# Optimization experiments

Hardware: AMD Instinct MI355X
Metric: run time of the kernel (lower is better)

## Reference

```python
import jax, jax.numpy as jnp
import numpy as np

G, K1, K2, N, NP, EPS = 16, 128, 32, 128, 512, 1e-5

def _bn(x, axes):
    m = jnp.mean(x, axes, keepdims=True)
    v = jnp.var(x, axes, keepdims=True)  # biased, as torch BN training mode
    return (x - m) * jax.lax.rsqrt(v + EPS)

def _fps(xyz, npoint):
    # farthest point sampling, deterministic start at index 0; xyz (B,P,3)
    B, P, _ = xyz.shape
    def step(carry, _):
        dists, far = carry
        c = jnp.take_along_axis(xyz, far[:, None, None], axis=1)   # (B,1,3)
        d = jnp.sum((xyz - c) ** 2, -1)                            # (B,P)
        dists = jnp.minimum(dists, d)
        return (dists, jnp.argmax(dists, -1)), far
    init = (jnp.full((B, P), 1e10, xyz.dtype), jnp.zeros((B,), jnp.int32))
    _, idx = jax.lax.scan(step, init, None, length=npoint)         # (npoint,B)
    return jnp.take_along_axis(xyz, idx.T[:, :, None], axis=1)     # (B,npoint,3)

def _pointnet(x, w1, b1, w2, b2, w3, b3):
    h = jax.nn.relu(_bn(x @ w1 + b1, (0, 1)))
    h = jax.nn.relu(_bn(h @ w2 + b2, (0, 1)))
    h = _bn(h @ w3 + b3, (0, 1))
    return jnp.max(h, axis=1)                                      # (B,1024)

def _mapping(feat, w1, b1, w2, b2, w3, b3, w4, b4):
    # all 16 branches stacked on leading axis g
    h = jax.nn.relu(_bn(jnp.einsum('bk,gkj->gbj', feat, w1) + b1[:, None, :], (1,)))
    h = jax.nn.relu(_bn(jnp.einsum('gbj,gjk->gbk', h, w2) + b2[:, None, :], (1,)))
    h = jax.nn.relu(_bn(jnp.einsum('gbj,gjk->gbk', h, w3) + b3[:, None, :], (1,)))
    return jax.nn.relu(_bn(jnp.einsum('gbj,gjk->gbk', h, w4) + b4[:, None, :], (1,)))

def _axform(feat, fw, fb, c1w, c1b, c2w, c2b, c3w, c3b, c4w, c4b):
    # feat (G,B,K1); 1x1 convs expressed as einsums in channels-last layout
    xb = (jnp.einsum('gbk,gkm->gbm', feat, fw) + fb[:, None, :]).reshape(G, -1, N, K2)
    h = jax.nn.relu(_bn(jnp.einsum('gbnk,gkc->gbnc', xb, c1w) + c1b[:, None, None, :], (1, 2)))
    h = jax.nn.relu(_bn(jnp.einsum('gbnc,gcd->gbnd', h, c2w) + c2b[:, None, None, :], (1, 2)))
    h = jnp.einsum('gbnd,gde->gbne', h, c3w) + c3b[:, None, None, :]  # (G,B,N,1024)
    w = jax.nn.softmax(h, axis=2)                                     # softmax over N
    y = jnp.einsum('gbne,gbnk->gbek', w, xb)                          # (G,B,1024,K2)
    return jnp.einsum('gbek,gkc->gbec', y, c4w) + c4b[:, None, None, :]  # (G,B,1024,3)

def _forward(x, pn, mp, gen, ref):
    x_partial = _fps(x, NP)                                           # (B,512,3)
    feat = _pointnet(x, *pn)                                          # (B,1024)
    mfeat = _mapping(feat, *mp)                                       # (G,B,K1)
    x1g = _axform(mfeat, *gen)                                        # (G,B,1024,3)
    B = x.shape[0]
    x_1 = jnp.transpose(x1g, (1, 0, 2, 3)).reshape(B, -1, 3)          # (B,16384,3)
    fps1 = jax.vmap(lambda p: _fps(p, NP))(x1g)                       # (G,B,512,3)
    x_base = jnp.concatenate([fps1, jnp.broadcast_to(x_partial, (G,) + x_partial.shape)], axis=2)
    x2g = x_base + _axform(mfeat, *ref)                               # (G,B,1024,3)
    x_2 = jnp.transpose(x2g, (1, 0, 2, 3)).reshape(B, -1, 3)
    return x_1, x_2

def setup_inputs() -> dict:
    keys = iter(jax.random.split(jax.random.key(0), 40))
    def rn(shape, s=0.02):
        return (s * jax.random.normal(next(keys), shape)).astype(jnp.float32)
    inp = {}
    inp['x'] = jax.random.normal(next(keys), (16, 2048, 3), jnp.float32)
    inp['pn_w1'] = rn((3, 64));      inp['pn_b1'] = rn((64,))
    inp['pn_w2'] = rn((64, 128));    inp['pn_b2'] = rn((128,))
    inp['pn_w3'] = rn((128, 1024));  inp['pn_b3'] = rn((1024,))
    inp['mp_w1'] = rn((G, 1024, 1024)); inp['mp_b1'] = rn((G, 1024))
    inp['mp_w2'] = rn((G, 1024, 1024)); inp['mp_b2'] = rn((G, 1024))
    inp['mp_w3'] = rn((G, 1024, 1024)); inp['mp_b3'] = rn((G, 1024))
    inp['mp_w4'] = rn((G, 1024, K1));   inp['mp_b4'] = rn((G, K1))
    for p in ('g', 'r'):
        inp[p + '_fw'] = rn((G, K1, N * K2)); inp[p + '_fb'] = rn((G, N * K2))
        inp[p + '_c1w'] = rn((G, K2, 64));    inp[p + '_c1b'] = rn((G, 64))
        inp[p + '_c2w'] = rn((G, 64, 128));   inp[p + '_c2b'] = rn((G, 128))
        inp[p + '_c3w'] = rn((G, 128, 1024)); inp[p + '_c3b'] = rn((G, 1024))
        inp[p + '_c4w'] = rn((G, K2, 3));     inp[p + '_c4b'] = rn((G, 3))
    return inp

def reference(x, pn_w1, pn_b1, pn_w2, pn_b2, pn_w3, pn_b3,
              mp_w1, mp_b1, mp_w2, mp_b2, mp_w3, mp_b3, mp_w4, mp_b4,
              g_fw, g_fb, g_c1w, g_c1b, g_c2w, g_c2b, g_c3w, g_c3b, g_c4w, g_c4b,
              r_fw, r_fb, r_c1w, r_c1b, r_c2w, r_c2b, r_c3w, r_c3b, r_c4w, r_c4b):
    pn = (pn_w1, pn_b1, pn_w2, pn_b2, pn_w3, pn_b3)
    mp = (mp_w1, mp_b1, mp_w2, mp_b2, mp_w3, mp_b3, mp_w4, mp_b4)
    gen = (g_fw, g_fb, g_c1w, g_c1b, g_c2w, g_c2b, g_c3w, g_c3b, g_c4w, g_c4b)
    ref = (r_fw, r_fb, r_c1w, r_c1b, r_c2w, r_c2b, r_c3w, r_c3b, r_c4w, r_c4b)
    return _forward(x, pn, mp, gen, ref)
```

## Files before the change

### kernel.cpp

```cpp
#include <hip/hip_runtime.h>
#include <math.h>

#define TID ((int)threadIdx.x)

namespace {
constexpr float EPSf = 1e-5f;

typedef __attribute__((ext_vector_type(8))) short short8;
typedef __attribute__((ext_vector_type(4))) float f32x4;

struct FpsArgs {
  const float* pts; float* out; float* dmin; int* far;
  int it0, it1, nc;
};

__device__ __forceinline__ unsigned fenc(float f){
  unsigned u = __float_as_uint(f);
  return (u & 0x80000000u) ? ~u : (u | 0x80000000u);
}
__device__ __forceinline__ float fdec(unsigned e){
  unsigned u = (e & 0x80000000u) ? (e & 0x7fffffffu) : ~e;
  return __uint_as_float(u);
}
__device__ __forceinline__ short bf16rne(float f){
  unsigned u = __float_as_uint(f);
  return (short)((u + 0x7fffu + ((u >> 16) & 1u)) >> 16);
}

template<int CTRL>
__device__ __forceinline__ void dpp_comb(float& bm, int& bp){
  int om_i = __builtin_amdgcn_update_dpp(__float_as_int(bm), __float_as_int(bm), CTRL, 0xf, 0xf, false);
  int op   = __builtin_amdgcn_update_dpp(bp, bp, CTRL, 0xf, 0xf, false);
  float om = __int_as_float(om_i);
  if (om > bm || (om == bm && op < bp)){ bm = om; bp = op; }
}

template<int LP, int NT>
__device__ void fps_body(const FpsArgs& a, int ci){
  const int NPTS = NT*LP;
  const float* pts = a.pts + (size_t)ci * NPTS * 3;
  float* out = a.out + (size_t)ci * 512 * 3;
  float* dst = a.dmin + (size_t)ci * NPTS;
  float px[LP], py[LP], pz[LP], dmin[LP];
#pragma unroll
  for (int j = 0; j < LP; j++){
    int p = TID + NT*j;
    px[j] = pts[p*3+0]; py[j] = pts[p*3+1]; pz[j] = pts[p*3+2];
  }
  int far;
  if (a.it0 == 0){
#pragma unroll
    for (int j = 0; j < LP; j++) dmin[j] = 1e10f;
    far = 0;
  } else {
#pragma unroll
    for (int j = 0; j < LP; j++) dmin[j] = dst[TID + NT*j];
    far = a.far[ci];
  }
  __shared__ unsigned long long red2[2][NT/64];
  for (int i = a.it0; i < a.it1; i++){
    float cx = pts[far*3+0], cy = pts[far*3+1], cz = pts[far*3+2];
    if (TID == 0){ out[i*3+0]=cx; out[i*3+1]=cy; out[i*3+2]=cz; }
    float bm = -1.f; int bp = 0;
#pragma unroll
    for (int j = 0; j < LP; j++){
      float dx = __fsub_rn(px[j], cx);
      float dy = __fsub_rn(py[j], cy);
      float dz = __fsub_rn(pz[j], cz);
      float d  = __fadd_rn(__fadd_rn(__fmul_rn(dx,dx), __fmul_rn(dy,dy)), __fmul_rn(dz,dz));
      float dm = fminf(dmin[j], d);
      dmin[j] = dm;
      if (dm > bm){ bm = dm; bp = TID + NT*j; }
    }
    dpp_comb<0x111>(bm,bp); dpp_comb<0x112>(bm,bp); dpp_comb<0x114>(bm,bp);
    dpp_comb<0x118>(bm,bp); dpp_comb<0x142>(bm,bp); dpp_comb<0x143>(bm,bp);
    unsigned long long key =
      ((unsigned long long)(unsigned)__builtin_amdgcn_readlane(__float_as_int(bm), 63) << 32)
      | (unsigned)~(unsigned)__builtin_amdgcn_readlane(bp, 63);
    if ((TID & 63) == 63) red2[i&1][TID>>6] = key;
    __syncthreads();
    unsigned long long kk = red2[i&1][0];
#pragma unroll
    for (int t = 1; t < NT/64; t++){
      unsigned long long o = red2[i&1][t];
      kk = kk > o ? kk : o;
    }
    far = (int)~(unsigned)kk;
  }
  if (a.it1 < 512){
#pragma unroll
    for (int j = 0; j < LP; j++) dst[TID + NT*j] = dmin[j];
    if (TID == 0) a.far[ci] = far;
  }
}

__device__ __forceinline__ int pswz(int n, int e){
  return (n << 6) + (e ^ (((n >> 3) & 3) << 3) ^ ((n >> 5) & 3));
}

template<int C, int K, int FLP>
__global__ void __launch_bounds__(256) rowgemm_kernel(const float* __restrict__ in,
    const float* __restrict__ w, const float* __restrict__ bias, const float2* __restrict__ st2,
    float* __restrict__ out, int rows_per_g, FpsArgs fa)
{
  int bid = blockIdx.x;
  if constexpr (FLP > 0){
    if (bid < fa.nc){ fps_body<FLP,256>(fa, bid); return; }
    bid -= fa.nc;
  }
  constexpr int RPB = 256 / C;
  __shared__ float lin[RPB * K];
  size_t row0 = (size_t)bid * RPB;
  int g = (int)(row0 / rows_per_g);
  for (int i = TID; i < RPB*K; i += 256){
    float v = in[row0*(size_t)K + i];
    if (st2){ float2 s = st2[(size_t)g*K + (i % K)]; v = fmaxf((v - s.x)*s.y, 0.f); }
    lin[i] = v;
  }
  __syncthreads();
  int r = TID / C, c = TID % C;
  float acc = bias[(size_t)g*C + c];
  const float* wg = w + (size_t)g*K*C + c;
#pragma unroll
  for (int k = 0; k < K; k++) acc = fmaf(lin[r*K + k], wg[(size_t)k*C], acc);
  out[(row0 + r)*C + c] = acc;
}

template<int FLP>
__global__ void __launch_bounds__(256, 4) big1024b_kernel(const float* __restrict__ in,
    const float* __restrict__ w, const float* __restrict__ bias, const float2* __restrict__ st2,
    float* __restrict__ ps, float* __restrict__ pq, unsigned* __restrict__ maxenc, FpsArgs fa)
{
  int bid = blockIdx.x;
  if constexpr (FLP > 0){
    if (bid < fa.nc){ fps_body<FLP,256>(fa, bid); return; }
    bid -= fa.nc;
  }
  int rb = bid >> 1, ch = bid & 1;
  size_t row0 = (size_t)rb * 32;
  __shared__ float linT[4096];
  for (int i = TID; i < 4096; i += 256){
    int r = i >> 7, k = i & 127;
    float v = in[(row0 + r)*128 + k];
    float2 s = st2[k];
    linT[k*32 + r] = fmaxf((v - s.x)*s.y, 0.f);
  }
  __syncthreads();
  int rq = TID >> 6, cq = TID & 63;
  int c0 = ch*512 + cq*8;
  float acc[8][8];
  {
    float4 b0 = *(const float4*)(bias + c0);
    float4 b1 = *(const float4*)(bias + c0 + 4);
    const float bv[8] = {b0.x,b0.y,b0.z,b0.w,b1.x,b1.y,b1.z,b1.w};
#pragma unroll
    for (int ri = 0; ri < 8; ri++)
#pragma unroll
      for (int ci = 0; ci < 8; ci++) acc[ri][ci] = bv[ci];
  }
  const float* wp = w + c0;
#pragma unroll 2
  for (int k = 0; k < 128; k++){
    float4 w0 = *(const float4*)(wp + (size_t)k*1024);
    float4 w1 = *(const float4*)(wp + (size_t)k*1024 + 4);
    float4 l0 = *(const float4*)&linT[k*32 + rq*8];
    float4 l1 = *(const float4*)&linT[k*32 + rq*8 + 4];
    const float lv[8] = {l0.x,l0.y,l0.z,l0.w,l1.x,l1.y,l1.z,l1.w};
    const float wv[8] = {w0.x,w0.y,w0.z,w0.w,w1.x,w1.y,w1.z,w1.w};
#pragma unroll
    for (int ri = 0; ri < 8; ri++)
#pragma unroll
      for (int ci = 0; ci < 8; ci++)
        acc[ri][ci] = fmaf(lv[ri], wv[ci], acc[ri][ci]);
  }
  float s[8], q[8], m[8];
#pragma unroll
  for (int ci = 0; ci < 8; ci++){
    s[ci] = 0.f; q[ci] = 0.f; m[ci] = -1e38f;
#pragma unroll
    for (int ri = 0; ri < 8; ri++){
      float v = acc[ri][ci];
      s[ci] += v; q[ci] = fmaf(v, v, q[ci]); m[ci] = fmaxf(m[ci], v);
    }
  }
  __syncthreads();
  float* red = linT;
#pragma unroll
  for (int ci = 0; ci < 8; ci++){
    red[rq*512 + cq*8 + ci]        = s[ci];
    red[2048 + rq*512 + cq*8 + ci] = q[ci];
  }
  __syncthreads();
  if (rq == 0){
#pragma unroll
    for (int ci = 0; ci < 8; ci++){
      float ss = 0.f, qq = 0.f;
#pragma unroll
      for (int r = 0; r < 4; r++){
        ss += red[r*512 + cq*8 + ci];
        qq += red[2048 + r*512 + cq*8 + ci];
      }
      ps[(size_t)rb*1024 + c0 + ci] = ss;
      pq[(size_t)rb*1024 + c0 + ci] = qq;
    }
  }
  __syncthreads();
#pragma unroll
  for (int ci = 0; ci < 8; ci++) red[rq*512 + cq*8 + ci] = m[ci];
  __syncthreads();
  if (rq == 0){
    int b = (int)(row0 / 2048);
#pragma unroll
    for (int ci = 0; ci < 8; ci++){
      float mm = red[cq*8 + ci];
#pragma unroll
      for (int r = 1; r < 4; r++) mm = fmaxf(mm, red[r*512 + cq*8 + ci]);
      atomicMax(&maxenc[(size_t)b*1024 + c0 + ci], fenc(mm));
    }
  }
}

template<int FLP>
__global__ void __launch_bounds__(128) mapgemm2_kernel(const float* __restrict__ in, int in_gstride,
    const float* __restrict__ w, const float* __restrict__ bias, const float2* __restrict__ st2,
    float* __restrict__ out, int K, int J, int JB, int NS, FpsArgs fa)
{
  int bid = blockIdx.x;
  if constexpr (FLP > 0){
    if (bid < fa.nc){ fps_body<FLP,128>(fa, bid); return; }
    bid -= fa.nc;
  }
  int kc = bid / (JB*16);
  int g  = (bid / JB) % 16;
  int jb = bid % JB;
  int kchunk = K / NS, k0 = kc*kchunk;
  __shared__ float linT[128*16];
  const float* ing = in + (size_t)g * in_gstride;
  for (int i = TID; i < kchunk*16; i += 128){
    int b = i / kchunk, k = i - b*kchunk;
    float v = ing[(size_t)b*K + k0 + k];
    if (st2){ float2 s = st2[(size_t)g*K + k0 + k]; v = fmaxf((v - s.x)*s.y, 0.f); }
    linT[k*16 + b] = v;
  }
  __syncthreads();
  int bh = TID >> 6, jq = TID & 63;
  int j = jb*256 + jq*4;
  const float* wp = w + ((size_t)g*K + k0)*J + j;
  float4 a4[8];
#pragma unroll
  for (int bi = 0; bi < 8; bi++) a4[bi] = make_float4(0.f,0.f,0.f,0.f);
#pragma unroll 4
  for (int k = 0; k < kchunk; k++){
    float4 wv = *(const float4*)(wp + (size_t)k*J);
    float4 l0 = *(const float4*)&linT[k*16 + bh*8];
    float4 l1 = *(const float4*)&linT[k*16 + bh*8 + 4];
    const float lv[8] = {l0.x,l0.y,l0.z,l0.w,l1.x,l1.y,l1.z,l1.w};
#pragma unroll
    for (int bi = 0; bi < 8; bi++){
      a4[bi].x = fmaf(lv[bi], wv.x, a4[bi].x);
      a4[bi].y = fmaf(lv[bi], wv.y, a4[bi].y);
      a4[bi].z = fmaf(lv[bi], wv.z, a4[bi].z);
      a4[bi].w = fmaf(lv[bi], wv.w, a4[bi].w);
    }
  }
  if (NS == 1){
    float4 bv = *(const float4*)(bias + (size_t)g*J + j);
#pragma unroll
    for (int bi = 0; bi < 8; bi++){
      int b = bh*8 + bi;
      float4 o = make_float4(a4[bi].x+bv.x, a4[bi].y+bv.y, a4[bi].z+bv.z, a4[bi].w+bv.w);
      *(float4*)&out[((size_t)g*16 + b)*J + j] = o;
    }
  } else {
#pragma unroll
    for (int bi = 0; bi < 8; bi++)
      *(float4*)&out[(((size_t)kc*16 + g)*16 + bh*8 + bi)*J + j] = a4[bi];
  }
}

__global__ void __launch_bounds__(256) mapgemm_kernel(const float* __restrict__ in, int in_gstride,
    const float* __restrict__ w, const float* __restrict__ bias, const float2* __restrict__ st2,
    float* __restrict__ out, int K, int J, int JB, int NS)
{
  int bid = blockIdx.x;
  int kc = bid / (JB*16);
  int g  = (bid / JB) % 16;
  int jb = bid % JB;
  int j  = jb*256 + TID;
  bool jv = j < J;
  int jc = jv ? j : 0;
  int kchunk = K / NS;
  int k0 = kc * kchunk;
  __shared__ float lin[16 * 128];
  const float* ing = in + (size_t)g * in_gstride;
  float acc[16];
  float bv = (NS == 1 && jv) ? bias[(size_t)g*J + jc] : 0.f;
#pragma unroll
  for (int b = 0; b < 16; b++) acc[b] = bv;
  for (int kt = k0; kt < k0 + kchunk; kt += 128){
    __syncthreads();
    for (int i = TID; i < 2048; i += 256){
      int b = i >> 7, k = i & 127;
      float v = ing[(size_t)b*K + kt + k];
      if (st2){ float2 s = st2[(size_t)g*K + kt + k]; v = fmaxf((v - s.x)*s.y, 0.f); }
      lin[i] = v;
    }
    __syncthreads();
    const float* wg = w + ((size_t)g*K + kt)*J + jc;
    for (int k = 0; k < 128; k++){
      float wv = wg[(size_t)k*J];
#pragma unroll
      for (int b = 0; b < 16; b++) acc[b] = fmaf(lin[b*128 + k], wv, acc[b]);
    }
  }
  if (jv){
    if (NS == 1){
      for (int b = 0; b < 16; b++) out[((size_t)g*16 + b)*J + j] = acc[b];
    } else {
      for (int b = 0; b < 16; b++) out[(((size_t)kc*16 + g)*16 + b)*J + j] = acc[b];
    }
  }
}

__global__ void __launch_bounds__(256) redstats_kernel(const float* __restrict__ part,
    const float* __restrict__ bias, float* __restrict__ out, float2* __restrict__ st2,
    int J, int NS)
{
  int t = blockIdx.x*256 + TID;
  int g = t / J, j = t % J;
  float bv = bias[t];
  float s = 0.f, q = 0.f;
  for (int b = 0; b < 16; b++){
    float v = bv;
    for (int c = 0; c < NS; c++) v += part[(((size_t)c*16 + g)*16 + b)*J + j];
    out[((size_t)g*16 + b)*J + j] = v;
    s += v; q = fmaf(v, v, q);
  }
  float mean = s * (1.f/16.f);
  float var  = q * (1.f/16.f) - mean*mean;
  st2[t] = make_float2(mean, rsqrtf(fmaxf(var, 0.f) + EPSf));
}

template<int FLP>
__global__ void __launch_bounds__(256) statsacc_kernel(const float* __restrict__ in,
    float* __restrict__ part, int C, size_t chunk, FpsArgs fa)
{
  int bid = blockIdx.x;
  if constexpr (FLP > 0){
    if (bid < fa.nc){ fps_body<FLP,256>(fa, bid); return; }
    bid -= fa.nc;
  }
  size_t base = (size_t)bid * chunk;
  int c = TID % C;
  float s = 0.f, q = 0.f;
  for (size_t idx = base + TID; idx < base + chunk; idx += 256){
    float v = in[idx]; s += v; q = fmaf(v, v, q);
  }
  __shared__ float ls[256], lq[256];
  ls[TID] = s; lq[TID] = q; __syncthreads();
  if (TID < C){
    for (int t = TID + C; t < 256; t += C){ s += ls[t]; q += lq[t]; }
    part[((size_t)bid*C + c)*2]   = s;
    part[((size_t)bid*C + c)*2+1] = q;
  }
}

__global__ void statsfin_kernel(const float* __restrict__ part, float2* __restrict__ st2,
    int C, int G, float invR)
{
  int slot = blockIdx.x*256 + TID;
  if (slot >= G*C) return;
  int g = slot / C, c = slot % C;
  int bpg = 256 / G;
  float s = 0.f, q = 0.f;
  for (int b = 0; b < bpg; b++){
    size_t p = ((size_t)(g*bpg + b)*C + c)*2;
    s += part[p]; q += part[p+1];
  }
  float mean = s*invR;
  float var  = q*invR - mean*mean;
  st2[slot] = make_float2(mean, rsqrtf(fmaxf(var, 0.f) + EPSf));
}

__global__ void pnfin_kernel(const float* __restrict__ ps, const float* __restrict__ pq,
                             float2* __restrict__ st)
{
  int c = blockIdx.x*256 + TID;
  float s = 0.f, q = 0.f;
  for (int rb = 0; rb < 1024; rb++){ s += ps[rb*1024 + c]; q += pq[rb*1024 + c]; }
  float mean = s * (1.f/32768.f);
  float var  = q * (1.f/32768.f) - mean*mean;
  st[c] = make_float2(mean, rsqrtf(fmaxf(var, 0.f) + EPSf));
}

__global__ void feat_kernel(const unsigned* __restrict__ me, const float2* __restrict__ st,
                            float* __restrict__ feat)
{
  int t = blockIdx.x*256 + TID;
  int c = t & 1023;
  float2 s = st[c];
  feat[t] = (fdec(me[t]) - s.x) * s.y;
}

__global__ void __launch_bounds__(256) wtr_kernel(const float* __restrict__ c3w,
                                                  short* __restrict__ wt)
{
  int g = blockIdx.x >> 4, kt = blockIdx.x & 15;
  __shared__ float lds[8*1024];
  const float* src = c3w + ((size_t)g*128 + kt*8)*1024;
  for (int i = TID; i < 8192; i += 256) lds[i] = src[i];
  __syncthreads();
  for (int e = TID; e < 1024; e += 256){
    short8 v;
#pragma unroll
    for (int j = 0; j < 8; j++) v[j] = bf16rne(lds[j*1024 + e]);
    *(short8*)&wt[((size_t)g*1024 + e)*128 + kt*8] = v;
  }
}

template<int FLP>
__global__ void __launch_bounds__(256, 4) fused_kernel(const float* __restrict__ c2o,
    const float2* __restrict__ st2, const short* __restrict__ wt,
    const float* __restrict__ xb, const float* __restrict__ c4w, const float* __restrict__ c4b,
    float* __restrict__ out_pts, float* __restrict__ out_x1, FpsArgs fa)
{
  int bid = blockIdx.x;
  if constexpr (FLP > 0){
    if (bid < fa.nc){ fps_body<FLP,256>(fa, bid); return; }
    bid -= fa.nc;
  }
  int gb = bid >> 3, eb = bid & 7;
  int g = gb >> 4, b = gb & 15;
  __shared__ short Abf[16384];
  __shared__ float xbl[4096];
  float* Ps = (float*)Abf;

  for (int i = TID; i < 1024; i += 256){
    int n = i >> 3, q = i & 7;
    float4 v = *(const float4*)(xb + (size_t)gb*4096 + n*32 + q*4);
    *(float4*)&xbl[n*32 + ((q ^ ((n>>5)&3))<<2)] = v;
  }
  const float* src = c2o + (size_t)gb*16384;
  for (int i = TID; i < 2048; i += 256){
    int n = i >> 4, kc = i & 15;
    float4 a0 = *(const float4*)(src + n*128 + kc*8);
    float4 a1 = *(const float4*)(src + n*128 + kc*8 + 4);
    const float vals[8] = {a0.x,a0.y,a0.z,a0.w,a1.x,a1.y,a1.z,a1.w};
    short8 ob;
#pragma unroll
    for (int j = 0; j < 8; j++){
      float2 s = st2[(size_t)g*128 + kc*8 + j];
      ob[j] = bf16rne(fmaxf((vals[j] - s.x)*s.y, 0.f));
    }
    *(short8*)&Abf[n*128 + ((kc ^ (n & 7)) << 3)] = ob;
  }
  __syncthreads();

  int lane = TID & 63, wid = TID >> 6;
  int lr = lane & 15, lkg = lane >> 4;
  f32x4 acc[2][8];
#pragma unroll
  for (int nt = 0; nt < 2; nt++)
#pragma unroll
    for (int et = 0; et < 8; et++) acc[nt][et] = (f32x4){0.f,0.f,0.f,0.f};

  const short* wtg = wt + ((size_t)g*1024 + eb*128)*128;
#pragma unroll
  for (int kt = 0; kt < 4; kt++){
    int kb = kt*32 + lkg*8;
    int kcf = kb >> 3;
    short8 afr[2];
#pragma unroll
    for (int nt = 0; nt < 2; nt++){
      int row = wid*32 + nt*16 + lr;
      afr[nt] = *(const short8*)&Abf[row*128 + ((kcf ^ (row & 7)) << 3)];
    }
#pragma unroll
    for (int et = 0; et < 8; et++){
      short8 bfr = *(const short8*)&wtg[(et*16 + lr)*128 + kb];
      acc[0][et] = __builtin_amdgcn_mfma_f32_16x16x32_bf16(afr[0], bfr, acc[0][et], 0, 0, 0);
      acc[1][et] = __builtin_amdgcn_mfma_f32_16x16x32_bf16(afr[1], bfr, acc[1][et], 0, 0, 0);
    }
  }
  __syncthreads();

  for (int p = 0; p < 2; p++){
    if (p) __syncthreads();
#pragma unroll
    for (int nt = 0; nt < 2; nt++)
#pragma unroll
      for (int t = 0; t < 4; t++){
        int et = p*4 + t;
#pragma unroll
        for (int r = 0; r < 4; r++){
          int n = wid*32 + nt*16 + lkg*4 + r;
          Ps[pswz(n, t*16 + lr)] = acc[nt][et][r];
        }
      }
    __syncthreads();
    int el = TID >> 2, hq = TID & 3;
    float m = -1e38f;
    for (int j = 0; j < 32; j++) m = fmaxf(m, Ps[pswz(hq*32 + j, el)]);
    m = fmaxf(m, __shfl_xor(m, 1));
    m = fmaxf(m, __shfl_xor(m, 2));
    float s = 0.f;
    float4 y[8];
#pragma unroll
    for (int q = 0; q < 8; q++) y[q] = make_float4(0.f,0.f,0.f,0.f);
    for (int j = 0; j < 32; j++){
      int n = hq*32 + j;
      float wv = __expf(Ps[pswz(n, el)] - m);
      s += wv;
#pragma unroll
      for (int q = 0; q < 8; q++){
        float4 xv = *(const float4*)&xbl[n*32 + ((q ^ hq) << 2)];
        y[q].x = fmaf(wv, xv.x, y[q].x);
        y[q].y = fmaf(wv, xv.y, y[q].y);
        y[q].z = fmaf(wv, xv.z, y[q].z);
        y[q].w = fmaf(wv, xv.w, y[q].w);
      }
    }
    s += __shfl_xor(s, 1); s += __shfl_xor(s, 2);
#pragma unroll
    for (int q = 0; q < 8; q++){
      y[q].x += __shfl_xor(y[q].x, 1); y[q].x += __shfl_xor(y[q].x, 2);
      y[q].y += __shfl_xor(y[q].y, 1); y[q].y += __shfl_xor(y[q].y, 2);
      y[q].z += __shfl_xor(y[q].z, 1); y[q].z += __shfl_xor(y[q].z, 2);
      y[q].w += __shfl_xor(y[q].w, 1); y[q].w += __shfl_xor(y[q].w, 2);
    }
    if (hq == 0){
      const float* cw = c4w + g*96;
      float o0 = 0.f, o1 = 0.f, o2 = 0.f;
#pragma unroll
      for (int q = 0; q < 8; q++){
#pragma unroll
        for (int c2 = 0; c2 < 4; c2++){
          float yv = (&y[q].x)[c2];
          int k = q*4 + c2;
          o0 = fmaf(yv, cw[k*3+0], o0);
          o1 = fmaf(yv, cw[k*3+1], o1);
          o2 = fmaf(yv, cw[k*3+2], o2);
        }
      }
      float rs = 1.f / s;
      o0 = fmaf(rs, o0, c4b[g*3+0]);
      o1 = fmaf(rs, o1, c4b[g*3+1]);
      o2 = fmaf(rs, o2, c4b[g*3+2]);
      int eg = eb*128 + p*64 + el;
      size_t po = ((size_t)gb*1024 + eg)*3;
      out_pts[po+0] = o0; out_pts[po+1] = o1; out_pts[po+2] = o2;
      if (out_x1){
        size_t xo = (((size_t)b*16 + g)*1024 + eg)*3;
        out_x1[xo+0] = o0; out_x1[xo+1] = o1; out_x1[xo+2] = o2;
      }
    }
  }
}

__global__ void combine_kernel(const float* __restrict__ fps1, const float* __restrict__ xpart,
                               const float* __restrict__ d2, float* __restrict__ x2)
{
  size_t i = (size_t)blockIdx.x*256 + TID;
  if (i >= (size_t)16*16*1024*3) return;
  int c = (int)(i % 3);
  size_t t = i / 3;
  int e = (int)(t % 1024);
  size_t gb = t / 1024;
  int g = (int)(gb >> 4), b = (int)(gb & 15);
  float base;
  if (e < 512) base = fps1[(gb*512 + e)*3 + c];
  else         base = xpart[((size_t)b*512 + (e - 512))*3 + c];
  x2[(((size_t)b*16384) + (size_t)g*1024 + e)*3 + c] = base + d2[i];
}

}

extern "C" void kernel_launch(void* const* d_in, const int* in_sizes, int n_in,
                              void* d_out, int out_size, void* d_ws, size_t ws_size,
                              hipStream_t stream)
{
  (void)in_sizes; (void)n_in; (void)out_size; (void)ws_size;
  const float* x    = (const float*)d_in[0];
  const float* pnw1 = (const float*)d_in[1];
  const float* pnb1 = (const float*)d_in[2];
  const float* pnw2 = (const float*)d_in[3];
  const float* pnb2 = (const float*)d_in[4];
  const float* pnw3 = (const float*)d_in[5];
  const float* pnb3 = (const float*)d_in[6];
  const float* mpw[4] = {(const float*)d_in[7],(const float*)d_in[9],(const float*)d_in[11],(const float*)d_in[13]};
  const float* mpb[4] = {(const float*)d_in[8],(const float*)d_in[10],(const float*)d_in[12],(const float*)d_in[14]};

  float* ws = (float*)d_ws;
  size_t o = 0;
  auto alloc = [&](size_t n){ float* p = ws + o; o += n; return p; };
  float* x_partial = alloc(24576);
  float* feat      = alloc(16384);
  float* mfeat     = alloc(32768);
  float2* st_pn1   = (float2*)alloc(128);
  float2* st_pn2   = (float2*)alloc(256);
  float2* st_pn3   = (float2*)alloc(2048);
  float2* st_c1    = (float2*)alloc(2048);
  float2* st_c2    = (float2*)alloc(4096);
  float2* st_map0  = (float2*)alloc(32768);
  float2* st_map1  = (float2*)alloc(32768);
  float2* st_map2  = (float2*)alloc(32768);
  float2* st_map3  = (float2*)alloc(4096);
  float* sa_part   = alloc(65536);
  float* pn_ps     = alloc(1048576);
  float* pn_pq     = alloc(1048576);
  unsigned* maxenc = (unsigned*)alloc(16384);
  float* mapA      = alloc(262144);
  float* mapB      = alloc(262144);
  float* mpart     = alloc(4194304);
  float* xb        = alloc(1048576);
  float* c1o       = alloc(2097152);
  float* c2o       = alloc(4194304);
  float* x1g       = alloc(786432);
  float* d2buf     = alloc(786432);
  float* fps1b     = alloc(393216);
  float* fpsA_dmin = alloc(32768);
  int*   fpsA_far  = (int*)alloc(16);
  float* fpsB_dmin = alloc(262144);
  int*   fpsB_far  = (int*)alloc(256);
  short* wt_g      = (short*)alloc(1048576);
  short* wt_r      = (short*)alloc(1048576);

  float* xout1 = (float*)d_out;
  float* xout2 = xout1 + 786432;

  hipMemsetAsync(maxenc, 0, 16384*sizeof(unsigned), stream);

  wtr_kernel<<<256, 256, 0, stream>>>((const float*)d_in[21], wt_g);
  wtr_kernel<<<256, 256, 0, stream>>>((const float*)d_in[31], wt_r);

  FpsArgs f0{};
  FpsArgs fa{x, x_partial, fpsA_dmin, fpsA_far, 0, 0, 16};

  fa.it0 = 0; fa.it1 = 64;
  rowgemm_kernel<64,3,8><<<8192+16, 256, 0, stream>>>(x, pnw1, pnb1, nullptr, c1o, 32768, fa);
  statsacc_kernel<0><<<256, 256, 0, stream>>>(c1o, sa_part, 64, 8192, f0);
  statsfin_kernel<<<1, 256, 0, stream>>>(sa_part, st_pn1, 64, 1, 1.f/32768.f);
  fa.it0 = 64; fa.it1 = 128;
  rowgemm_kernel<128,64,8><<<16384+16, 256, 0, stream>>>(c1o, pnw2, pnb2, st_pn1, c2o, 32768, fa);
  statsacc_kernel<0><<<256, 256, 0, stream>>>(c2o, sa_part, 128, 16384, f0);
  statsfin_kernel<<<1, 256, 0, stream>>>(sa_part, st_pn2, 128, 1, 1.f/32768.f);
  fa.it0 = 128; fa.it1 = 224;
  big1024b_kernel<8><<<2048+16, 256, 0, stream>>>(c2o, pnw3, pnb3, st_pn2,
                                                  pn_ps, pn_pq, maxenc, fa);
  pnfin_kernel<<<4, 256, 0, stream>>>(pn_ps, pn_pq, st_pn3);
  feat_kernel<<<64, 256, 0, stream>>>(maxenc, st_pn3, feat);

  fa.it0 = 224; fa.it1 = 288;
  mapgemm2_kernel<16><<<1024+16, 128, 0, stream>>>(feat, 0,     mpw[0], nullptr, nullptr, mpart, 1024, 1024, 4, 16, fa);
  redstats_kernel<<<64, 256, 0, stream>>>(mpart, mpb[0], mapA, st_map0, 1024, 16);
  fa.it0 = 288; fa.it1 = 352;
  mapgemm2_kernel<16><<<1024+16, 128, 0, stream>>>(mapA, 16384, mpw[1], nullptr, st_map0, mpart, 1024, 1024, 4, 16, fa);
  redstats_kernel<<<64, 256, 0, stream>>>(mpart, mpb[1], mapB, st_map1, 1024, 16);
  fa.it0 = 352; fa.it1 = 416;
  mapgemm2_kernel<16><<<1024+16, 128, 0, stream>>>(mapB, 16384, mpw[2], nullptr, st_map1, mpart, 1024, 1024, 4, 16, fa);
  redstats_kernel<<<64, 256, 0, stream>>>(mpart, mpb[2], mapA, st_map2, 1024, 16);
  mapgemm_kernel<<<64, 256, 0, stream>>>(mapA, 16384, mpw[3], nullptr, st_map2, mpart, 1024, 128, 1, 4);
  redstats_kernel<<<8, 256, 0, stream>>>(mpart, mpb[3], mfeat, st_map3, 128, 4);

  for (int p = 0; p < 2; p++){
    const float* fw  = (const float*)d_in[15 + p*10 + 0];
    const float* fb  = (const float*)d_in[15 + p*10 + 1];
    const float* c1w = (const float*)d_in[15 + p*10 + 2];
    const float* c1b = (const float*)d_in[15 + p*10 + 3];
    const float* c2w = (const float*)d_in[15 + p*10 + 4];
    const float* c2b = (const float*)d_in[15 + p*10 + 5];
    const float* c4w = (const float*)d_in[15 + p*10 + 8];
    const float* c4b = (const float*)d_in[15 + p*10 + 9];

    if (p == 0){
      fa.it0 = 416; fa.it1 = 480;
      mapgemm2_kernel<16><<<256+16, 128, 0, stream>>>(mfeat, 2048, fw, fb, st_map3, xb, 128, 4096, 16, 1, fa);
      fa.it0 = 480; fa.it1 = 512;
      rowgemm_kernel<64,32,8><<<8192+16, 256, 0, stream>>>(xb, c1w, c1b, nullptr, c1o, 2048, fa);
      statsacc_kernel<0><<<256, 256, 0, stream>>>(c1o, sa_part, 64, 8192, f0);
      statsfin_kernel<<<4, 256, 0, stream>>>(sa_part, st_c1, 64, 16, 1.f/2048.f);
      rowgemm_kernel<128,64,0><<<16384, 256, 0, stream>>>(c1o, c2w, c2b, st_c1, c2o, 2048, f0);
      statsacc_kernel<0><<<256, 256, 0, stream>>>(c2o, sa_part, 128, 16384, f0);
      statsfin_kernel<<<8, 256, 0, stream>>>(sa_part, st_c2, 128, 16, 1.f/2048.f);
      fused_kernel<0><<<2048, 256, 0, stream>>>(c2o, st_c2, wt_g, xb, c4w, c4b, x1g, xout1, f0);
    } else {
      FpsArgs fb_{x1g, fps1b, fpsB_dmin, fpsB_far, 0, 0, 256};
      mapgemm2_kernel<0><<<256, 128, 0, stream>>>(mfeat, 2048, fw, fb, st_map3, xb, 128, 4096, 16, 1, f0);
      fb_.it0 = 0; fb_.it1 = 72;
      rowgemm_kernel<64,32,4><<<8192+256, 256, 0, stream>>>(xb, c1w, c1b, nullptr, c1o, 2048, fb_);
      fb_.it0 = 72; fb_.it1 = 104;
      statsacc_kernel<4><<<256+256, 256, 0, stream>>>(c1o, sa_part, 64, 8192, fb_);
      statsfin_kernel<<<4, 256, 0, stream>>>(sa_part, st_c1, 64, 16, 1.f/2048.f);
      fb_.it0 = 104; fb_.it1 = 208;
      rowgemm_kernel<128,64,4><<<16384+256, 256, 0, stream>>>(c1o, c2w, c2b, st_c1, c2o, 2048, fb_);
      fb_.it0 = 208; fb_.it1 = 240;
      statsacc_kernel<4><<<256+256, 256, 0, stream>>>(c2o, sa_part, 128, 16384, fb_);
      statsfin_kernel<<<8, 256, 0, stream>>>(sa_part, st_c2, 128, 16, 1.f/2048.f);
      fb_.it0 = 240; fb_.it1 = 512;
      fused_kernel<4><<<2048+256, 256, 0, stream>>>(c2o, st_c2, wt_r, xb, c4w, c4b, d2buf, nullptr, fb_);
    }
  }

  combine_kernel<<<3072, 256, 0, stream>>>(fps1b, x_partial, d2buf, xout2);
}
```

Baseline: 1.853 ms.

## Compute softmax in registers and apply weights via bf16 MFMA

The fused attention-like kernel no longer spills logits to LDS for a scalar softmax and FMA-based weighted sum. It computes the max and sum across the N dimension from MFMA accumulators using cross-lane shuffles plus a small LDS reduction, writes exponentiated weights as bf16, and computes the weighted sum of xb with a second bf16 MFMA. xb is stored transposed in bf16. This removes the scalar inner loops over N, at the cost of extra bf16 rounding on the softmax weights and xb, and a lower occupancy hint in the launch bounds.

```diff
diff --git a/kernel.cpp b/kernel.cpp
--- a/kernel.cpp
+++ b/kernel.cpp
@@ -92,10 +92,6 @@
     for (int j = 0; j < LP; j++) dst[TID + NT*j] = dmin[j];
     if (TID == 0) a.far[ci] = far;
   }
-}
-
-__device__ __forceinline__ int pswz(int n, int e){
-  return (n << 6) + (e ^ (((n >> 3) & 3) << 3) ^ ((n >> 5) & 3));
 }
 
 template<int C, int K, int FLP>
@@ -419,7 +415,7 @@
 }
 
 template<int FLP>
-__global__ void __launch_bounds__(256, 4) fused_kernel(const float* __restrict__ c2o,
+__global__ void __launch_bounds__(256, 3) fused_kernel(const float* __restrict__ c2o,
     const float2* __restrict__ st2, const short* __restrict__ wt,
     const float* __restrict__ xb, const float* __restrict__ c4w, const float* __restrict__ c4b,
     float* __restrict__ out_pts, float* __restrict__ out_x1, FpsArgs fa)
@@ -432,13 +428,22 @@
   int gb = bid >> 3, eb = bid & 7;
   int g = gb >> 4, b = gb & 15;
   __shared__ short Abf[16384];
-  __shared__ float xbl[4096];
-  float* Ps = (float*)Abf;
-
-  for (int i = TID; i < 1024; i += 256){
-    int n = i >> 3, q = i & 7;
-    float4 v = *(const float4*)(xb + (size_t)gb*4096 + n*32 + q*4);
-    *(float4*)&xbl[n*32 + ((q ^ ((n>>5)&3))<<2)] = v;
+  __shared__ short xbT[4096];
+  __shared__ float mred[512];
+  __shared__ float sred[128];
+
+  {
+    const float* xsrc = xb + (size_t)gb*4096;
+    for (int idx = TID; idx < 1024; idx += 256){
+      int n = idx >> 3, k4 = (idx & 7)*4;
+      float4 v = *(const float4*)(xsrc + n*32 + k4);
+      const float vv[4] = {v.x, v.y, v.z, v.w};
+#pragma unroll
+      for (int j = 0; j < 4; j++){
+        int k = k4 + j;
+        xbT[k*128 + (((n >> 3) ^ (k & 7)) << 3) + (n & 7)] = bf16rne(vv[j]);
+      }
+    }
   }
   const float* src = c2o + (size_t)gb*16384;
   for (int i = TID; i < 2048; i += 256){
@@ -458,12 +463,12 @@
 
   int lane = TID & 63, wid = TID >> 6;
   int lr = lane & 15, lkg = lane >> 4;
+
   f32x4 acc[2][8];
 #pragma unroll
   for (int nt = 0; nt < 2; nt++)
 #pragma unroll
     for (int et = 0; et < 8; et++) acc[nt][et] = (f32x4){0.f,0.f,0.f,0.f};
-
   const short* wtg = wt + ((size_t)g*1024 + eb*128)*128;
 #pragma unroll
   for (int kt = 0; kt < 4; kt++){
@@ -482,76 +487,132 @@
       acc[1][et] = __builtin_amdgcn_mfma_f32_16x16x32_bf16(afr[1], bfr, acc[1][et], 0, 0, 0);
     }
   }
-  __syncthreads();
-
-  for (int p = 0; p < 2; p++){
-    if (p) __syncthreads();
+
+  float m[8];
+#pragma unroll
+  for (int et = 0; et < 8; et++){
+    float mm = -1e38f;
 #pragma unroll
     for (int nt = 0; nt < 2; nt++)
 #pragma unroll
-      for (int t = 0; t < 4; t++){
-        int et = p*4 + t;
-#pragma unroll
-        for (int r = 0; r < 4; r++){
-          int n = wid*32 + nt*16 + lkg*4 + r;
-          Ps[pswz(n, t*16 + lr)] = acc[nt][et][r];
+      for (int r = 0; r < 4; r++) mm = fmaxf(mm, acc[nt][et][r]);
+    mm = fmaxf(mm, __shfl_xor(mm, 16));
+    mm = fmaxf(mm, __shfl_xor(mm, 32));
+    m[et] = mm;
+  }
+  if (lkg == 0){
+#pragma unroll
+    for (int et = 0; et < 8; et++) mred[wid*128 + et*16 + lr] = m[et];
+  }
+  __syncthreads();
+#pragma unroll
+  for (int et = 0; et < 8; et++){
+    float mm = fmaxf(fmaxf(mred[et*16 + lr],       mred[128 + et*16 + lr]),
+                     fmaxf(mred[256 + et*16 + lr], mred[384 + et*16 + lr]));
+    m[et] = mm;
+  }
+
+  float sp[8];
+  unsigned* Pu = (unsigned*)Abf;
+#pragma unroll
+  for (int et = 0; et < 8; et++){
+    float ss = 0.f;
+#pragma unroll
+    for (int nt = 0; nt < 2; nt++)
+#pragma unroll
+      for (int r = 0; r < 4; r++){
+        float p = __expf(acc[nt][et][r] - m[et]);
+        acc[nt][et][r] = p;
+        ss += p;
+      }
+    ss += __shfl_xor(ss, 16);
+    ss += __shfl_xor(ss, 32);
+    sp[et] = ss;
+    int e = et*16 + lr;
+#pragma unroll
+    for (int nt = 0; nt < 2; nt++){
+      int nb = wid*32 + nt*16 + lkg*4;
+      int base = e*128 + ((((nb >> 3)) ^ (e & 7)) << 3) + (nb & 7);
+      unsigned lo = (unsigned)(unsigned short)bf16rne(acc[nt][et][0])
+                  | ((unsigned)(unsigned short)bf16rne(acc[nt][et][1]) << 16);
+      unsigned hi = (unsigned)(unsigned short)bf16rne(acc[nt][et][2])
+                  | ((unsigned)(unsigned short)bf16rne(acc[nt][et][3]) << 16);
+      Pu[base >> 1]       = lo;
+      Pu[(base >> 1) + 1] = hi;
+    }
+  }
+  __syncthreads();
+  if (lkg == 0){
+#pragma unroll
+    for (int et = 0; et < 8; et++) mred[wid*128 + et*16 + lr] = sp[et];
+  }
+  __syncthreads();
+  if (wid == 0){
+#pragma unroll
+    for (int t = 0; t < 2; t++){
+      int e = t*64 + lane;
+      float s = mred[e] + mred[128 + e] + mred[256 + e] + mred[384 + e];
+      sred[e] = 1.f / s;
+    }
+  }
+
+  f32x4 yy[2][2];
+#pragma unroll
+  for (int t2 = 0; t2 < 2; t2++){ yy[t2][0] = (f32x4){0.f,0.f,0.f,0.f}; yy[t2][1] = (f32x4){0.f,0.f,0.f,0.f}; }
+#pragma unroll
+  for (int nc = 0; nc < 4; nc++){
+    short8 bfrs[2];
+#pragma unroll
+    for (int kt2 = 0; kt2 < 2; kt2++){
+      int k = kt2*16 + lr;
+      bfrs[kt2] = *(const short8*)&xbT[k*128 + (((nc*4 + lkg) ^ (k & 7)) << 3)];
+    }
+#pragma unroll
+    for (int t2 = 0; t2 < 2; t2++){
+      int e = (wid*2 + t2)*16 + lr;
+      short8 afr = *(const short8*)&Abf[e*128 + (((nc*4 + lkg) ^ (e & 7)) << 3)];
+      yy[t2][0] = __builtin_amdgcn_mfma_f32_16x16x32_bf16(afr, bfrs[0], yy[t2][0], 0, 0, 0);
+      yy[t2][1] = __builtin_amdgcn_mfma_f32_16x16x32_bf16(afr, bfrs[1], yy[t2][1], 0, 0, 0);
+    }
+  }
+  __syncthreads();
+
+  float c4l[2][3];
+  {
+    const float* cw = c4w + g*96;
+#pragma unroll
+    for (int kt2 = 0; kt2 < 2; kt2++){
+      int k = kt2*16 + lr;
+      c4l[kt2][0] = cw[k*3+0]; c4l[kt2][1] = cw[k*3+1]; c4l[kt2][2] = cw[k*3+2];
+    }
+  }
+  float cb0 = c4b[g*3+0], cb1 = c4b[g*3+1], cb2 = c4b[g*3+2];
+#pragma unroll
+  for (int t2 = 0; t2 < 2; t2++){
+#pragma unroll
+    for (int r = 0; r < 4; r++){
+      float o0 = yy[t2][0][r]*c4l[0][0] + yy[t2][1][r]*c4l[1][0];
+      float o1 = yy[t2][0][r]*c4l[0][1] + yy[t2][1][r]*c4l[1][1];
+      float o2 = yy[t2][0][r]*c4l[0][2] + yy[t2][1][r]*c4l[1][2];
+#pragma unroll
+      for (int d = 1; d < 16; d <<= 1){
+        o0 += __shfl_xor(o0, d);
+        o1 += __shfl_xor(o1, d);
+        o2 += __shfl_xor(o2, d);
+      }
+      if (lr == 0){
+        int e = (wid*2 + t2)*16 + lkg*4 + r;
+        float rs = sred[e];
+        o0 = fmaf(o0, rs, cb0);
+        o1 = fmaf(o1, rs, cb1);
+        o2 = fmaf(o2, rs, cb2);
+        int eg = eb*128 + e;
+        size_t po = ((size_t)gb*1024 + eg)*3;
+        out_pts[po+0] = o0; out_pts[po+1] = o1; out_pts[po+2] = o2;
+        if (out_x1){
+          size_t xo = (((size_t)b*16 + g)*1024 + eg)*3;
+          out_x1[xo+0] = o0; out_x1[xo+1] = o1; out_x1[xo+2] = o2;
         }
-      }
-    __syncthreads();
-    int el = TID >> 2, hq = TID & 3;
-    float m = -1e38f;
-    for (int j = 0; j < 32; j++) m = fmaxf(m, Ps[pswz(hq*32 + j, el)]);
-    m = fmaxf(m, __shfl_xor(m, 1));
-    m = fmaxf(m, __shfl_xor(m, 2));
-    float s = 0.f;
-    float4 y[8];
-#pragma unroll
-    for (int q = 0; q < 8; q++) y[q] = make_float4(0.f,0.f,0.f,0.f);
-    for (int j = 0; j < 32; j++){
-      int n = hq*32 + j;
-      float wv = __expf(Ps[pswz(n, el)] - m);
-      s += wv;
-#pragma unroll
-      for (int q = 0; q < 8; q++){
-        float4 xv = *(const float4*)&xbl[n*32 + ((q ^ hq) << 2)];
-        y[q].x = fmaf(wv, xv.x, y[q].x);
-        y[q].y = fmaf(wv, xv.y, y[q].y);
-        y[q].z = fmaf(wv, xv.z, y[q].z);
-        y[q].w = fmaf(wv, xv.w, y[q].w);
-      }
-    }
-    s += __shfl_xor(s, 1); s += __shfl_xor(s, 2);
-#pragma unroll
-    for (int q = 0; q < 8; q++){
-      y[q].x += __shfl_xor(y[q].x, 1); y[q].x += __shfl_xor(y[q].x, 2);
-      y[q].y += __shfl_xor(y[q].y, 1); y[q].y += __shfl_xor(y[q].y, 2);
-      y[q].z += __shfl_xor(y[q].z, 1); y[q].z += __shfl_xor(y[q].z, 2);
-      y[q].w += __shfl_xor(y[q].w, 1); y[q].w += __shfl_xor(y[q].w, 2);
-    }
-    if (hq == 0){
-      const float* cw = c4w + g*96;
-      float o0 = 0.f, o1 = 0.f, o2 = 0.f;
-#pragma unroll
-      for (int q = 0; q < 8; q++){
-#pragma unroll
-        for (int c2 = 0; c2 < 4; c2++){
-          float yv = (&y[q].x)[c2];
-          int k = q*4 + c2;
-          o0 = fmaf(yv, cw[k*3+0], o0);
-          o1 = fmaf(yv, cw[k*3+1], o1);
-          o2 = fmaf(yv, cw[k*3+2], o2);
-        }
-      }
-      float rs = 1.f / s;
-      o0 = fmaf(rs, o0, c4b[g*3+0]);
-      o1 = fmaf(rs, o1, c4b[g*3+1]);
-      o2 = fmaf(rs, o2, c4b[g*3+2]);
-      int eg = eb*128 + p*64 + el;
-      size_t po = ((size_t)gb*1024 + eg)*3;
-      out_pts[po+0] = o0; out_pts[po+1] = o1; out_pts[po+2] = o2;
-      if (out_x1){
-        size_t xo = (((size_t)b*16 + g)*1024 + eg)*3;
-        out_x1[xo+0] = o0; out_x1[xo+1] = o1; out_x1[xo+2] = o2;
       }
     }
   }
```

Measured after the change: 1.794 ms. -3.2%, faster.
